# Optimization experiments

Hardware: AMD Instinct MI355X
Metric: run time of the kernel (lower is better)

## Reference

```python
import jax, jax.numpy as jnp
import numpy as np

N_GROUP = 8
TOPK_GROUP = 4
TOP_K = 8
ROUTED_SCALING = 2.5
NUM_EXPERTS = 256
HIDDEN = 7168
TOKENS = 8192


def setup_inputs() -> dict:
    key = jax.random.key(0)
    k1, k2, k3 = jax.random.split(key, 3)
    hidden_states = jax.random.normal(k1, (TOKENS, HIDDEN), dtype=jnp.float32)
    weight = jax.random.normal(k2, (NUM_EXPERTS, HIDDEN), dtype=jnp.float32) * 0.02
    e_score_correction_bias = jax.random.normal(k3, (NUM_EXPERTS,), dtype=jnp.float32) * 0.1
    return {"hidden_states": hidden_states, "weight": weight,
            "e_score_correction_bias": e_score_correction_bias}


def reference(hidden_states, weight, e_score_correction_bias):
    # logits = x @ W^T  (fp32 gate GEMM)
    logits = jnp.einsum('th,eh->te', hidden_states.astype(jnp.float32), weight)
    scores = jax.nn.sigmoid(logits)                       # [T, E]
    swb = scores + e_score_correction_bias                # [T, E]
    T, E = swb.shape
    gsize = E // N_GROUP
    # per-group score = sum of top-2 biased scores within each group
    grouped = swb.reshape(T, N_GROUP, gsize)
    top2, _ = jax.lax.top_k(grouped, 2)                   # [T, G, 2]
    group_scores = top2.sum(axis=-1)                      # [T, G]
    # keep topk_group groups
    _, gidx = jax.lax.top_k(group_scores, TOPK_GROUP)     # [T, topk_group]
    rows = jnp.arange(T)[:, None]
    group_mask = jnp.zeros((T, N_GROUP), jnp.float32).at[rows, gidx].set(1.0)
    score_mask = jnp.repeat(group_mask, gsize, axis=-1)   # [T, E]
    swb_masked = swb * score_mask
    # top_k experts among kept groups
    _, tidx = jax.lax.top_k(swb_masked, TOP_K)            # [T, top_k]
    new_mask = jnp.zeros((T, E), jnp.float32).at[rows, tidx].set(1.0)
    sel = scores * new_mask
    score_sum = sel.sum(axis=-1, keepdims=True) + 1e-20
    return sel / score_sum * ROUTED_SCALING
```

## Files before the change

### kernel.cpp

```cpp
#include <hip/hip_runtime.h>
#include <math.h>

#define TOKENS   8192
#define HIDDEN   7168
#define NEXPERT  256
#define NGROUP   8
#define TOPKG    4
#define TOPK     8
#define SCALE    2.5f

#define BM 128
#define BN 128
#define BK 32
#define KSPLIT 8
#define KPB (HIDDEN / KSPLIT)
#define NT  (KPB / BK)
#define TILE_BYTES 16384

#define RSTR 72

typedef _Float16 half8 __attribute__((ext_vector_type(8)));
typedef _Float16 half4 __attribute__((ext_vector_type(4)));
typedef float    floatx4 __attribute__((ext_vector_type(4)));

__device__ __forceinline__ void cvt_store(_Float16* __restrict__ H,
                                          int row, int k0, float4 v) {
    half4 h, l;
    h[0] = (_Float16)v.x; h[1] = (_Float16)v.y;
    h[2] = (_Float16)v.z; h[3] = (_Float16)v.w;
    l[0] = (_Float16)(v.x - (float)h[0]);
    l[1] = (_Float16)(v.y - (float)h[1]);
    l[2] = (_Float16)(v.z - (float)h[2]);
    l[3] = (_Float16)(v.w - (float)h[3]);
    const int base = row * RSTR + ((k0 >> 3) << 4) + (k0 & 7);
    *(half4*)&H[base]     = h;
    *(half4*)&H[base + 8] = l;
}

__device__ __forceinline__ void cvt8(const float4 a, const float4 b,
                                     half8& h, half8& l) {
    h[0] = (_Float16)a.x; h[1] = (_Float16)a.y;
    h[2] = (_Float16)a.z; h[3] = (_Float16)a.w;
    h[4] = (_Float16)b.x; h[5] = (_Float16)b.y;
    h[6] = (_Float16)b.z; h[7] = (_Float16)b.w;
    l[0] = (_Float16)(a.x - (float)h[0]); l[1] = (_Float16)(a.y - (float)h[1]);
    l[2] = (_Float16)(a.z - (float)h[2]); l[3] = (_Float16)(a.w - (float)h[3]);
    l[4] = (_Float16)(b.x - (float)h[4]); l[5] = (_Float16)(b.y - (float)h[5]);
    l[6] = (_Float16)(b.z - (float)h[6]); l[7] = (_Float16)(b.w - (float)h[7]);
}

__global__ __launch_bounds__(896) void wsplit_kernel(
    const float* __restrict__ W, char* __restrict__ WS, float* __restrict__ O)
{
    const int gt = blockIdx.x * 896 + threadIdx.x;
#pragma unroll
    for (int i = 0; i < 3; i++) {
        const int idx = gt + i * (NEXPERT * 896);
        if (idx < TOKENS * NEXPERT / 4)
            *(float4*)&O[(size_t)idx * 4] = float4{0.f, 0.f, 0.f, 0.f};
    }

    const int e  = blockIdx.x;
    const int og = threadIdx.x;
    const float4 a = *(const float4*)&W[(size_t)e * HIDDEN + og * 8];
    const float4 b = *(const float4*)&W[(size_t)e * HIDDEN + og * 8 + 4];
    half8 h, l;
    cvt8(a, b, h, l);

    const int kz = og / (KPB / 8);
    const int tt = (og % (KPB / 8)) >> 2;
    const int oc = og & 3;
    const int row = e & 127, nb = e >> 7;
    char* p = WS + (size_t)((nb * KSPLIT + kz) * NT + tt) * TILE_BYTES
            + (row * 4 + oc) * 32;
    *(half8*)p        = h;
    *(half8*)(p + 16) = l;
}

__global__ __launch_bounds__(256, 4) void gate_gemm_kernel(
    const float* __restrict__ X, const char* __restrict__ WS,
    float* __restrict__ OUT)
{
    __shared__ _Float16 Ab[BM * RSTR];
    __shared__ _Float16 Bb[BN * RSTR];

    const int tid = threadIdx.x;
    const int nb  = blockIdx.x * BN;
    const int mb  = blockIdx.y * BM;
    const int kb  = blockIdx.z * KPB;

    const int srow = tid >> 3;
    const int sk0  = (tid & 7) * 4;
    const float* Aptr = X + (size_t)(mb + srow) * HIDDEN + kb + sk0;

    const char* Wimg =
        WS + (size_t)((blockIdx.x * KSPLIT + blockIdx.z) * NT) * TILE_BYTES;
    const int bbase[2] = { (tid >> 2) * RSTR + (tid & 3) * 16,
                           ((tid >> 2) + 64) * RSTR + (tid & 3) * 16 };

    float4 av[4];
    half8  nh[2], nl[2];
#pragma unroll
    for (int q = 0; q < 4; q++)
        av[q] = *(const float4*)(Aptr + (size_t)(q * 32) * HIDDEN);
#pragma unroll
    for (int s = 0; s < 2; s++) {
        const char* src = Wimg + (tid + 256 * s) * 32;
        nh[s] = *(const half8*)src;
        nl[s] = *(const half8*)(src + 16);
    }

    const int lane = tid & 63, wave = tid >> 6;
    const int wm = (wave >> 1) * 64, wn = (wave & 1) * 64;
    const int fr = lane & 15, quad = lane >> 4;

    floatx4 acc[4][4];
#pragma unroll
    for (int i = 0; i < 4; i++)
#pragma unroll
        for (int j = 0; j < 4; j++) acc[i][j] = floatx4{0.f, 0.f, 0.f, 0.f};

    for (int t = 0; t < NT; t++) {
#pragma unroll
        for (int q = 0; q < 4; q++)
            cvt_store(Ab, q * 32 + srow, sk0, av[q]);
#pragma unroll
        for (int s = 0; s < 2; s++) {
            *(half8*)&Bb[bbase[s]]     = nh[s];
            *(half8*)&Bb[bbase[s] + 8] = nl[s];
        }

        __syncthreads();

        if (t + 1 < NT) {
            const int o = (t + 1) * BK;
#pragma unroll
            for (int q = 0; q < 4; q++)
                av[q] = *(const float4*)(Aptr + o + (size_t)(q * 32) * HIDDEN);
            const char* srcT = Wimg + (size_t)(t + 1) * TILE_BYTES;
#pragma unroll
            for (int s = 0; s < 2; s++) {
                const char* src = srcT + (tid + 256 * s) * 32;
                nh[s] = *(const half8*)src;
                nl[s] = *(const half8*)(src + 16);
            }
        }

        half8 ah[4], al[4];
#pragma unroll
        for (int i = 0; i < 4; i++) {
            const int a = (wm + i * 16 + fr) * RSTR + quad * 16;
            ah[i] = *(const half8*)&Ab[a];
            al[i] = *(const half8*)&Ab[a + 8];
        }
#pragma unroll
        for (int j = 0; j < 4; j++) {
            const int b = (wn + j * 16 + fr) * RSTR + quad * 16;
            const half8 bh = *(const half8*)&Bb[b];
            const half8 bl = *(const half8*)&Bb[b + 8];
#pragma unroll
            for (int i = 0; i < 4; i++) {
                acc[i][j] = __builtin_amdgcn_mfma_f32_16x16x32_f16(
                    al[i], bh, acc[i][j], 0, 0, 0);
                acc[i][j] = __builtin_amdgcn_mfma_f32_16x16x32_f16(
                    ah[i], bl, acc[i][j], 0, 0, 0);
                acc[i][j] = __builtin_amdgcn_mfma_f32_16x16x32_f16(
                    ah[i], bh, acc[i][j], 0, 0, 0);
            }
        }

        __syncthreads();
    }

#pragma unroll
    for (int i = 0; i < 4; i++)
#pragma unroll
        for (int j = 0; j < 4; j++) {
            const int col = nb + wn + j * 16 + fr;
#pragma unroll
            for (int r = 0; r < 4; r++) {
                const int row = mb + wm + i * 16 + quad * 4 + r;
                atomicAdd(&OUT[(size_t)row * NEXPERT + col], acc[i][j][r]);
            }
        }
}

__global__ __launch_bounds__(256) void route_kernel(
    float* __restrict__ S, const float* __restrict__ bias)
{
    const int lane = threadIdx.x & 63;
    const int wave = threadIdx.x >> 6;
    const int t    = blockIdx.x * 4 + wave;

    const float4 lg4 = *(const float4*)&S[(size_t)t * NEXPERT + lane * 4];
    const float4 b4  = *(const float4*)&bias[lane * 4];
    float sc[4];
    sc[0] = 1.0f / (1.0f + expf(-lg4.x));
    sc[1] = 1.0f / (1.0f + expf(-lg4.y));
    sc[2] = 1.0f / (1.0f + expf(-lg4.z));
    sc[3] = 1.0f / (1.0f + expf(-lg4.w));
    float swb[4] = { sc[0] + b4.x, sc[1] + b4.y, sc[2] + b4.z, sc[3] + b4.w };

    float m1 = -INFINITY, m2 = -INFINITY;
#pragma unroll
    for (int j = 0; j < 4; j++) {
        const float v = swb[j];
        if (v > m1)      { m2 = m1; m1 = v; }
        else if (v > m2) { m2 = v; }
    }
#pragma unroll
    for (int s = 1; s < 8; s <<= 1) {
        const float o1 = __shfl_xor(m1, s, 64);
        const float o2 = __shfl_xor(m2, s, 64);
        const float hi = fmaxf(m1, o1);
        const float lo = fminf(m1, o1);
        m2 = fmaxf(lo, fmaxf(m2, o2));
        m1 = hi;
    }
    const float gs = m1 + m2;

    float gsc[NGROUP];
#pragma unroll
    for (int g = 0; g < NGROUP; g++) gsc[g] = __shfl(gs, g * 8, 64);
    const int myg = lane >> 3;
    int rank = 0;
#pragma unroll
    for (int g = 0; g < NGROUP; g++)
        rank += (gsc[g] > gs) || (gsc[g] == gs && g < myg);
    const bool kept = (rank < TOPKG);

    float v[4];
#pragma unroll
    for (int j = 0; j < 4; j++) v[j] = kept ? swb[j] : 0.0f;

    float sum = 0.0f;
    int selmask = 0;
    for (int r = 0; r < TOPK; r++) {
        float bv = -INFINITY;
        int   bi = 0x7fffffff;
#pragma unroll
        for (int j = 0; j < 4; j++) {
            const bool avail = ((selmask >> j) & 1) == 0;
            if (avail && v[j] > bv) { bv = v[j]; bi = lane * 4 + j; }
        }
#pragma unroll
        for (int s = 1; s < 64; s <<= 1) {
            const float ov = __shfl_xor(bv, s, 64);
            const int   oi = __shfl_xor(bi, s, 64);
            if (ov > bv || (ov == bv && oi < bi)) { bv = ov; bi = oi; }
        }
        const int wl = bi >> 2, wj = bi & 3;
        const float mysc = (wj == 0) ? sc[0] : (wj == 1) ? sc[1]
                         : (wj == 2) ? sc[2] : sc[3];
        sum += __shfl(mysc, wl, 64);
        if (lane == wl) selmask |= (1 << wj);
    }

    const float rcp = SCALE / (sum + 1e-20f);
    float4 o;
    o.x = (selmask & 1) ? sc[0] * rcp : 0.0f;
    o.y = (selmask & 2) ? sc[1] * rcp : 0.0f;
    o.z = (selmask & 4) ? sc[2] * rcp : 0.0f;
    o.w = (selmask & 8) ? sc[3] * rcp : 0.0f;
    *(float4*)&S[(size_t)t * NEXPERT + lane * 4] = o;
}

extern "C" void kernel_launch(void* const* d_in, const int* in_sizes, int n_in,
                              void* d_out, int out_size, void* d_ws, size_t ws_size,
                              hipStream_t stream) {
    const float* X    = (const float*)d_in[0];
    const float* W    = (const float*)d_in[1];
    const float* bias = (const float*)d_in[2];
    float* out = (float*)d_out;
    char* ws = (char*)d_ws; (void)ws_size;

    wsplit_kernel<<<NEXPERT, 896, 0, stream>>>(W, ws, out);
    dim3 ggrid(NEXPERT / BN, TOKENS / BM, KSPLIT);
    gate_gemm_kernel<<<ggrid, 256, 0, stream>>>(X, ws, out);
    route_kernel<<<TOKENS / 4, 256, 0, stream>>>(out, bias);
}
```

Baseline: 401.9 us.

## Load MFMA fragments directly from global, dropping LDS staging and syncs

Rewrites the gate GEMM so each wave loads its A (fp32, split to fp16 hi/lo in registers) and pre-split B fragments straight from global memory into registers, with register double-buffering instead of LDS staging and barriers. Each block now covers all 256 experts for 64 tokens, and the K split is reduced from 8 to 4, halving atomic output traffic. The weight pre-split layout is changed to match. The cost is that every wave redundantly loads the same A rows, and access patterns rely on caches instead of shared-memory reuse.

New measurement: 542.0 us. +34.8%, slower.

```diff
diff --git a/kernel.cpp b/kernel.cpp
--- a/kernel.cpp
+++ b/kernel.cpp
@@ -9,33 +9,15 @@
 #define TOPK     8
 #define SCALE    2.5f
 
-#define BM 128
-#define BN 128
+#define BM 64
 #define BK 32
-#define KSPLIT 8
+#define KSPLIT 4
 #define KPB (HIDDEN / KSPLIT)
 #define NT  (KPB / BK)
-#define TILE_BYTES 16384
-
-#define RSTR 72
+#define WTILE_BYTES 32768
 
 typedef _Float16 half8 __attribute__((ext_vector_type(8)));
-typedef _Float16 half4 __attribute__((ext_vector_type(4)));
 typedef float    floatx4 __attribute__((ext_vector_type(4)));
-
-__device__ __forceinline__ void cvt_store(_Float16* __restrict__ H,
-                                          int row, int k0, float4 v) {
-    half4 h, l;
-    h[0] = (_Float16)v.x; h[1] = (_Float16)v.y;
-    h[2] = (_Float16)v.z; h[3] = (_Float16)v.w;
-    l[0] = (_Float16)(v.x - (float)h[0]);
-    l[1] = (_Float16)(v.y - (float)h[1]);
-    l[2] = (_Float16)(v.z - (float)h[2]);
-    l[3] = (_Float16)(v.w - (float)h[3]);
-    const int base = row * RSTR + ((k0 >> 3) << 4) + (k0 & 7);
-    *(half4*)&H[base]     = h;
-    *(half4*)&H[base + 8] = l;
-}
 
 __device__ __forceinline__ void cvt8(const float4 a, const float4 b,
                                      half8& h, half8& l) {
@@ -70,49 +52,25 @@
     const int kz = og / (KPB / 8);
     const int tt = (og % (KPB / 8)) >> 2;
     const int oc = og & 3;
-    const int row = e & 127, nb = e >> 7;
-    char* p = WS + (size_t)((nb * KSPLIT + kz) * NT + tt) * TILE_BYTES
-            + (row * 4 + oc) * 32;
+    char* p = WS + (size_t)(kz * NT + tt) * WTILE_BYTES + (e * 4 + oc) * 32;
     *(half8*)p        = h;
     *(half8*)(p + 16) = l;
 }
 
-__global__ __launch_bounds__(256, 4) void gate_gemm_kernel(
+__global__ __launch_bounds__(256, 2) void gate_gemm_kernel(
     const float* __restrict__ X, const char* __restrict__ WS,
     float* __restrict__ OUT)
 {
-    __shared__ _Float16 Ab[BM * RSTR];
-    __shared__ _Float16 Bb[BN * RSTR];
-
-    const int tid = threadIdx.x;
-    const int nb  = blockIdx.x * BN;
-    const int mb  = blockIdx.y * BM;
-    const int kb  = blockIdx.z * KPB;
-
-    const int srow = tid >> 3;
-    const int sk0  = (tid & 7) * 4;
-    const float* Aptr = X + (size_t)(mb + srow) * HIDDEN + kb + sk0;
-
-    const char* Wimg =
-        WS + (size_t)((blockIdx.x * KSPLIT + blockIdx.z) * NT) * TILE_BYTES;
-    const int bbase[2] = { (tid >> 2) * RSTR + (tid & 3) * 16,
-                           ((tid >> 2) + 64) * RSTR + (tid & 3) * 16 };
-
-    float4 av[4];
-    half8  nh[2], nl[2];
-#pragma unroll
-    for (int q = 0; q < 4; q++)
-        av[q] = *(const float4*)(Aptr + (size_t)(q * 32) * HIDDEN);
-#pragma unroll
-    for (int s = 0; s < 2; s++) {
-        const char* src = Wimg + (tid + 256 * s) * 32;
-        nh[s] = *(const half8*)src;
-        nl[s] = *(const half8*)(src + 16);
-    }
-
+    const int tid  = threadIdx.x;
     const int lane = tid & 63, wave = tid >> 6;
-    const int wm = (wave >> 1) * 64, wn = (wave & 1) * 64;
-    const int fr = lane & 15, quad = lane >> 4;
+    const int mb   = blockIdx.x * BM;
+    const int kz   = blockIdx.y;
+    const int wn   = wave * 64;
+    const int fr   = lane & 15, quad = lane >> 4;
+
+    const float* Abase = X + (size_t)(mb + fr) * HIDDEN + kz * KPB + quad * 8;
+    const char* Bbase = WS + (size_t)(kz * NT) * WTILE_BYTES
+                      + (wn + fr) * 128 + quad * 32;
 
     floatx4 acc[4][4];
 #pragma unroll
@@ -120,66 +78,67 @@
 #pragma unroll
         for (int j = 0; j < 4; j++) acc[i][j] = floatx4{0.f, 0.f, 0.f, 0.f};
 
-    for (int t = 0; t < NT; t++) {
-#pragma unroll
-        for (int q = 0; q < 4; q++)
-            cvt_store(Ab, q * 32 + srow, sk0, av[q]);
-#pragma unroll
-        for (int s = 0; s < 2; s++) {
-            *(half8*)&Bb[bbase[s]]     = nh[s];
-            *(half8*)&Bb[bbase[s] + 8] = nl[s];
-        }
-
-        __syncthreads();
-
-        if (t + 1 < NT) {
-            const int o = (t + 1) * BK;
-#pragma unroll
-            for (int q = 0; q < 4; q++)
-                av[q] = *(const float4*)(Aptr + o + (size_t)(q * 32) * HIDDEN);
-            const char* srcT = Wimg + (size_t)(t + 1) * TILE_BYTES;
-#pragma unroll
-            for (int s = 0; s < 2; s++) {
-                const char* src = srcT + (tid + 256 * s) * 32;
-                nh[s] = *(const half8*)src;
-                nl[s] = *(const half8*)(src + 16);
-            }
-        }
-
-        half8 ah[4], al[4];
-#pragma unroll
-        for (int i = 0; i < 4; i++) {
-            const int a = (wm + i * 16 + fr) * RSTR + quad * 16;
-            ah[i] = *(const half8*)&Ab[a];
-            al[i] = *(const half8*)&Ab[a + 8];
-        }
+    float4 avA[4][2], avB[4][2];
+    half8  bhA[4], blA[4], bhB[4], blB[4];
+
+#pragma unroll
+    for (int i = 0; i < 4; i++) {
+        const float* ap = Abase + (size_t)(i * 16) * HIDDEN;
+        avA[i][0] = *(const float4*)ap;
+        avA[i][1] = *(const float4*)(ap + 4);
+    }
+#pragma unroll
+    for (int j = 0; j < 4; j++) {
+        bhA[j] = *(const half8*)(Bbase + j * 2048);
+        blA[j] = *(const half8*)(Bbase + j * 2048 + 16);
+    }
+
+#define STEP(AVC, AVN, BHC, BLC, BHN, BLN, T)                                 \
+    {                                                                         \
+        half8 ah[4], al[4];                                                   \
+        _Pragma("unroll")                                                     \
+        for (int i = 0; i < 4; i++)                                           \
+            cvt8(AVC[i][0], AVC[i][1], ah[i], al[i]);                         \
+        const int tn = ((T) + 1 < NT) ? (T) + 1 : NT - 1;                     \
+        _Pragma("unroll")                                                     \
+        for (int i = 0; i < 4; i++) {                                         \
+            const float* ap = Abase + (size_t)(i * 16) * HIDDEN + tn * BK;    \
+            AVN[i][0] = *(const float4*)ap;                                   \
+            AVN[i][1] = *(const float4*)(ap + 4);                             \
+        }                                                                     \
+        const char* bp = Bbase + (size_t)tn * WTILE_BYTES;                    \
+        _Pragma("unroll")                                                     \
+        for (int j = 0; j < 4; j++) {                                         \
+            BHN[j] = *(const half8*)(bp + j * 2048);                          \
+            BLN[j] = *(const half8*)(bp + j * 2048 + 16);                     \
+        }                                                                     \
+        _Pragma("unroll")                                                     \
+        for (int j = 0; j < 4; j++)                                           \
+            _Pragma("unroll")                                                 \
+            for (int i = 0; i < 4; i++) {                                     \
+                acc[i][j] = __builtin_amdgcn_mfma_f32_16x16x32_f16(           \
+                    al[i], BHC[j], acc[i][j], 0, 0, 0);                       \
+                acc[i][j] = __builtin_amdgcn_mfma_f32_16x16x32_f16(           \
+                    ah[i], BLC[j], acc[i][j], 0, 0, 0);                       \
+                acc[i][j] = __builtin_amdgcn_mfma_f32_16x16x32_f16(           \
+                    ah[i], BHC[j], acc[i][j], 0, 0, 0);                       \
+            }                                                                 \
+    }
+
+    for (int t = 0; t < NT; t += 2) {
+        STEP(avA, avB, bhA, blA, bhB, blB, t)
+        STEP(avB, avA, bhB, blB, bhA, blA, t + 1)
+    }
+#undef STEP
+
+#pragma unroll
+    for (int i = 0; i < 4; i++)
 #pragma unroll
         for (int j = 0; j < 4; j++) {
-            const int b = (wn + j * 16 + fr) * RSTR + quad * 16;
-            const half8 bh = *(const half8*)&Bb[b];
-            const half8 bl = *(const half8*)&Bb[b + 8];
-#pragma unroll
-            for (int i = 0; i < 4; i++) {
-                acc[i][j] = __builtin_amdgcn_mfma_f32_16x16x32_f16(
-                    al[i], bh, acc[i][j], 0, 0, 0);
-                acc[i][j] = __builtin_amdgcn_mfma_f32_16x16x32_f16(
-                    ah[i], bl, acc[i][j], 0, 0, 0);
-                acc[i][j] = __builtin_amdgcn_mfma_f32_16x16x32_f16(
-                    ah[i], bh, acc[i][j], 0, 0, 0);
-            }
-        }
-
-        __syncthreads();
-    }
-
-#pragma unroll
-    for (int i = 0; i < 4; i++)
-#pragma unroll
-        for (int j = 0; j < 4; j++) {
-            const int col = nb + wn + j * 16 + fr;
+            const int col = wn + j * 16 + fr;
 #pragma unroll
             for (int r = 0; r < 4; r++) {
-                const int row = mb + wm + i * 16 + quad * 4 + r;
+                const int row = mb + i * 16 + quad * 4 + r;
                 atomicAdd(&OUT[(size_t)row * NEXPERT + col], acc[i][j][r]);
             }
         }
@@ -275,7 +234,7 @@
     char* ws = (char*)d_ws; (void)ws_size;
 
     wsplit_kernel<<<NEXPERT, 896, 0, stream>>>(W, ws, out);
-    dim3 ggrid(NEXPERT / BN, TOKENS / BM, KSPLIT);
+    dim3 ggrid(TOKENS / BM, KSPLIT);
     gate_gemm_kernel<<<ggrid, 256, 0, stream>>>(X, ws, out);
     route_kernel<<<TOKENS / 4, 256, 0, stream>>>(out, bias);
 }
```
